# Kernel optimization log

Hardware: AMD Instinct MI355X
Metric: run time of the kernel (lower is better)

## Reference

```python
import jax, jax.numpy as jnp
import numpy as np
import math

D_MODEL = 1024
NUM_HEADS = 16
HEAD_DIM = D_MODEL // NUM_HEADS


def _xavier(key, out_f, in_f):
    limit = math.sqrt(6.0 / (in_f + out_f))
    return jax.random.uniform(key, (out_f, in_f), jnp.float32, -limit, limit)


def ternarize(w):
    # abs-mean threshold -> {-1, 0, +1}
    abs_mean = jnp.mean(jnp.abs(w))
    return jnp.where(jnp.abs(w) > abs_mean, jnp.sign(w), jnp.zeros_like(w))


def setup_inputs() -> dict:
    key = jax.random.key(0)
    kq, kk, kv, kwq, kwk, kwv, kwo = jax.random.split(key, 7)
    B, S = 2, 2048
    return {
        "query": jax.random.normal(kq, (B, S, D_MODEL), jnp.float32),
        "key": jax.random.normal(kk, (B, S, D_MODEL), jnp.float32),
        "value": jax.random.normal(kv, (B, S, D_MODEL), jnp.float32),
        "w_q": _xavier(kwq, D_MODEL, D_MODEL),
        "w_k": _xavier(kwk, D_MODEL, D_MODEL),
        "w_v": _xavier(kwv, D_MODEL, D_MODEL),
        "w_o": _xavier(kwo, D_MODEL, D_MODEL),
    }


def reference(query, key, value, w_q, w_k, w_v, w_o):
    B, S, _ = query.shape
    # ternary projections (F.linear: x @ W.T)
    q = query @ ternarize(w_q).T
    k = key @ ternarize(w_k).T
    v = value @ ternarize(w_v).T
    # [B, H, S, Dh]
    q = q.reshape(B, S, NUM_HEADS, HEAD_DIM).transpose(0, 2, 1, 3)
    k = k.reshape(B, -1, NUM_HEADS, HEAD_DIM).transpose(0, 2, 1, 3)
    v = v.reshape(B, -1, NUM_HEADS, HEAD_DIM).transpose(0, 2, 1, 3)
    scores = jnp.einsum("bhqd,bhkd->bhqk", q, k) / math.sqrt(HEAD_DIM)
    probs = jax.nn.softmax(scores, axis=-1)
    out = jnp.einsum("bhqk,bhkd->bhqd", probs, v)
    out = out.transpose(0, 2, 1, 3).reshape(B, S, D_MODEL)
    return out @ ternarize(w_o).T
```

## Files before the change

kernel.cpp:

```cpp
#include <hip/hip_runtime.h>
#include <cstdint>
#include <cstddef>

typedef __bf16 bfloat;
typedef __bf16 bf16x8 __attribute__((ext_vector_type(8)));
typedef __bf16 bf16x4 __attribute__((ext_vector_type(4)));
typedef float  f32x4  __attribute__((ext_vector_type(4)));

static constexpr int D  = 1024;
static constexpr int S  = 2048;
static constexpr int B  = 2;
static constexpr int H  = 16;
static constexpr int DH = 64;
static constexpr int M  = B * S;
static constexpr int WMAT_N = 1024 * 1024;

#define MFMA_BF16(a, b, c) __builtin_amdgcn_mfma_f32_16x16x32_bf16((a), (b), (c), 0, 0, 0)

__device__ __forceinline__ void gl_lds16(const void* g, void* l) {
  __builtin_amdgcn_global_load_lds(
      (const __attribute__((address_space(1))) void*)g,
      (__attribute__((address_space(3))) void*)l, 16, 0, 0);
}

__global__ void prep_kernel(const float* __restrict__ w0, const float* __restrict__ w1,
                            const float* __restrict__ w2, const float* __restrict__ w3,
                            const float* __restrict__ qx, const float* __restrict__ kx,
                            const float* __restrict__ vx, bfloat* __restrict__ qhi,
                            bfloat* __restrict__ qlo, bfloat* __restrict__ khi,
                            bfloat* __restrict__ klo, bfloat* __restrict__ vhi,
                            double* __restrict__ sums) {
  const int y = blockIdx.y;
  if (y < 4) {
    const float* w = (y == 0) ? w0 : (y == 1) ? w1 : (y == 2) ? w2 : w3;
    const float4* w4 = (const float4*)w;
    double s = 0.0;
    for (int i = blockIdx.x * blockDim.x + threadIdx.x; i < (WMAT_N / 4);
         i += gridDim.x * blockDim.x) {
      float4 v = w4[i];
      s += (double)fabsf(v.x) + (double)fabsf(v.y) + (double)fabsf(v.z) + (double)fabsf(v.w);
    }
    for (int off = 1; off < 64; off <<= 1) s += __shfl_xor(s, off, 64);
    __shared__ double ps[4];
    if ((threadIdx.x & 63) == 0) ps[threadIdx.x >> 6] = s;
    __syncthreads();
    if (threadIdx.x == 0) atomicAdd(&sums[y], ps[0] + ps[1] + ps[2] + ps[3]);
  } else {
    const int z = y - 4;
    const float* x = (z == 0) ? qx : (z == 1) ? kx : vx;
    bfloat* hi = (z == 0) ? qhi : (z == 1) ? khi : vhi;
    bfloat* lo = (z == 0) ? qlo : (z == 1) ? klo : nullptr;
    const int n8 = M * D / 8;
    const float4* x4 = (const float4*)x;
    for (int i = blockIdx.x * blockDim.x + threadIdx.x; i < n8;
         i += gridDim.x * blockDim.x) {
      float4 a = x4[2 * i], b = x4[2 * i + 1];
      float f[8] = {a.x, a.y, a.z, a.w, b.x, b.y, b.z, b.w};
      bf16x8 h;
#pragma unroll
      for (int j = 0; j < 8; j++) h[j] = (bfloat)f[j];
      *(bf16x8*)&hi[(size_t)i * 8] = h;
      if (z < 2) {
        bf16x8 l;
#pragma unroll
        for (int j = 0; j < 8; j++) l[j] = (bfloat)(f[j] - (float)h[j]);
        *(bf16x8*)&lo[(size_t)i * 8] = l;
      }
    }
  }
}

__global__ void tern_kernel(const float* __restrict__ w0, const float* __restrict__ w1,
                            const float* __restrict__ w2, const float* __restrict__ w3,
                            bfloat* __restrict__ o0, bfloat* __restrict__ o1,
                            bfloat* __restrict__ o2, bfloat* __restrict__ o3,
                            const double* __restrict__ sums) {
  int z = blockIdx.y;
  const float* w = (z == 0) ? w0 : (z == 1) ? w1 : (z == 2) ? w2 : w3;
  bfloat* o = (z == 0) ? o0 : (z == 1) ? o1 : (z == 2) ? o2 : o3;
  double thr = sums[z] * (1.0 / (double)WMAT_N);
  const float4* w4 = (const float4*)w;
  for (int i = blockIdx.x * blockDim.x + threadIdx.x; i < (WMAT_N / 4);
       i += gridDim.x * blockDim.x) {
    float4 v = w4[i];
    bf16x4 r;
    r[0] = (bfloat)(((double)fabsf(v.x) > thr) ? (v.x > 0.f ? 1.f : -1.f) : 0.f);
    r[1] = (bfloat)(((double)fabsf(v.y) > thr) ? (v.y > 0.f ? 1.f : -1.f) : 0.f);
    r[2] = (bfloat)(((double)fabsf(v.z) > thr) ? (v.z > 0.f ? 1.f : -1.f) : 0.f);
    r[3] = (bfloat)(((double)fabsf(v.w) > thr) ? (v.w > 0.f ? 1.f : -1.f) : 0.f);
    *(bf16x4*)&o[(size_t)i * 4] = r;
  }
}

__global__ __launch_bounds__(256) void qkv_gemm(
    const bfloat* __restrict__ xqh, const bfloat* __restrict__ xql,
    const bfloat* __restrict__ xkh, const bfloat* __restrict__ xkl,
    const bfloat* __restrict__ xvh, const bfloat* __restrict__ wqt,
    const bfloat* __restrict__ wkt, const bfloat* __restrict__ wvt,
    bfloat* __restrict__ qmh, bfloat* __restrict__ qml,
    bfloat* __restrict__ kmh, bfloat* __restrict__ kml, bfloat* __restrict__ vtr) {
  constexpr int K = D;
  constexpr int N = D;
  __shared__ __align__(16) bfloat As0[128 * 64];
  __shared__ __align__(16) bfloat As1[128 * 64];
  __shared__ __align__(16) bfloat Ws[128 * 64];

  const int z = blockIdx.z;
  const bfloat *A0, *A1 = nullptr, *Wm;
  bfloat *Oh = nullptr, *Ol = nullptr;
  float scale = 1.f;
  bool split;
  if (z == 0) {
    A0 = xqh; A1 = xql; Wm = wqt; Oh = qmh; Ol = qml;
    scale = 0.18033688f;
    split = true;
  } else if (z == 1) {
    A0 = xkh; A1 = xkl; Wm = wkt; Oh = kmh; Ol = kml; split = true;
  } else {
    A0 = xvh; Wm = wvt; split = false;
  }

  const int t = threadIdx.x;
  const int w = t >> 6, lane = t & 63;
  const int quad = lane >> 4, l16 = lane & 15;
  const int wm = w >> 1, wn = w & 1;
  const int m0 = blockIdx.y * 128, n0 = blockIdx.x * 128;

  f32x4 acc[4][4] = {};

  const int srr = lane >> 3;
  const int spc = lane & 7;

  for (int kk = 0; kk < K; kk += 64) {
#pragma unroll
    for (int g = 0; g < 4; g++) {
      int row = w * 32 + g * 8 + srr;
      int cl = spc ^ (row & 7);
      int lo = (w * 32 + g * 8) * 64;
      gl_lds16(A0 + (size_t)(m0 + row) * K + kk + cl * 8, As0 + lo);
      if (split) gl_lds16(A1 + (size_t)(m0 + row) * K + kk + cl * 8, As1 + lo);
      gl_lds16(Wm + (size_t)(n0 + row) * K + kk + cl * 8, Ws + lo);
    }
    __syncthreads();

#pragma unroll
    for (int kidx = 0; kidx < 2; kidx++) {
      bf16x8 bfrag[4], afrag[4];
#pragma unroll
      for (int nt = 0; nt < 4; nt++) {
        int r = wn * 64 + nt * 16 + l16;
        bfrag[nt] = *(const bf16x8*)&Ws[r * 64 + (((kidx * 4 + quad) ^ (r & 7)) * 8)];
      }
#pragma unroll
      for (int mt = 0; mt < 4; mt++) {
        int r = wm * 64 + mt * 16 + l16;
        afrag[mt] = *(const bf16x8*)&As0[r * 64 + (((kidx * 4 + quad) ^ (r & 7)) * 8)];
      }
#pragma unroll
      for (int mt = 0; mt < 4; mt++)
#pragma unroll
        for (int nt = 0; nt < 4; nt++)
          acc[mt][nt] = MFMA_BF16(afrag[mt], bfrag[nt], acc[mt][nt]);
      if (split) {
#pragma unroll
        for (int mt = 0; mt < 4; mt++) {
          int r = wm * 64 + mt * 16 + l16;
          afrag[mt] = *(const bf16x8*)&As1[r * 64 + (((kidx * 4 + quad) ^ (r & 7)) * 8)];
        }
#pragma unroll
        for (int mt = 0; mt < 4; mt++)
#pragma unroll
          for (int nt = 0; nt < 4; nt++)
            acc[mt][nt] = MFMA_BF16(afrag[mt], bfrag[nt], acc[mt][nt]);
      }
    }
    __syncthreads();
  }

#pragma unroll
  for (int mt = 0; mt < 4; mt++) {
#pragma unroll
    for (int nt = 0; nt < 4; nt++) {
      const int row = m0 + wm * 64 + mt * 16 + quad * 4;
      const int col = n0 + wn * 64 + nt * 16 + l16;
      if (split) {
#pragma unroll
        for (int rg = 0; rg < 4; rg++) {
          float vv = acc[mt][nt][rg] * scale;
          size_t idx = (size_t)(row + rg) * N + col;
          bfloat hh = (bfloat)vv;
          Oh[idx] = hh;
          Ol[idx] = (bfloat)(vv - (float)hh);
        }
      } else {
        int bb = row >> 11, s = row & (S - 1);
        int kk6 = s & 63;
        int pos = (kk6 & 3) | (((kk6 >> 4) & 1) << 2) | (((kk6 >> 2) & 3) << 3) |
                  ((kk6 >> 5) << 5);
        int sp = (s & ~63) | pos;
        bf16x4 pk;
#pragma unroll
        for (int rg = 0; rg < 4; rg++) pk[rg] = (bfloat)acc[mt][nt][rg];
        *(bf16x4*)&vtr[(size_t)bb * D * S + (size_t)col * S + sp] = pk;
      }
    }
  }
}

__global__ __launch_bounds__(256, 4) void gemm_wo(const bfloat* __restrict__ A,
                                                  const bfloat* __restrict__ Wm,
                                                  float* __restrict__ Cf) {
  constexpr int K = D;
  constexpr int N = D;
  __shared__ __align__(16) bfloat As[64 * 64];
  __shared__ __align__(16) bfloat Ws[64 * 64];

  const int t = threadIdx.x;
  const int w = t >> 6, lane = t & 63;
  const int quad = lane >> 4, l16 = lane & 15;
  const int wm = w >> 1, wn = w & 1;
  const int m0 = blockIdx.y * 64, n0 = blockIdx.x * 64;

  f32x4 acc[2][2] = {};

  const int srr = lane >> 3;
  const int spc = lane & 7;

  for (int kk = 0; kk < K; kk += 64) {
#pragma unroll
    for (int g = 0; g < 2; g++) {
      int row = w * 16 + g * 8 + srr;
      int cl = spc ^ (row & 7);
      int lo = (w * 16 + g * 8) * 64;
      gl_lds16(A + (size_t)(m0 + row) * K + kk + cl * 8, As + lo);
      gl_lds16(Wm + (size_t)(n0 + row) * K + kk + cl * 8, Ws + lo);
    }
    __syncthreads();

#pragma unroll
    for (int kidx = 0; kidx < 2; kidx++) {
      bf16x8 af[2], bfr[2];
#pragma unroll
      for (int i = 0; i < 2; i++) {
        int ar = wm * 32 + i * 16 + l16;
        af[i] = *(const bf16x8*)&As[ar * 64 + (((kidx * 4 + quad) ^ (ar & 7)) * 8)];
        int br = wn * 32 + i * 16 + l16;
        bfr[i] = *(const bf16x8*)&Ws[br * 64 + (((kidx * 4 + quad) ^ (br & 7)) * 8)];
      }
#pragma unroll
      for (int mt = 0; mt < 2; mt++)
#pragma unroll
        for (int nt = 0; nt < 2; nt++)
          acc[mt][nt] = MFMA_BF16(af[mt], bfr[nt], acc[mt][nt]);
    }
    __syncthreads();
  }

#pragma unroll
  for (int mt = 0; mt < 2; mt++) {
#pragma unroll
    for (int nt = 0; nt < 2; nt++) {
      const int row = m0 + wm * 32 + mt * 16 + quad * 4;
      const int col = n0 + wn * 32 + nt * 16 + l16;
#pragma unroll
      for (int rg = 0; rg < 4; rg++) Cf[(size_t)(row + rg) * N + col] = acc[mt][nt][rg];
    }
  }
}

__global__ __launch_bounds__(256) void flash_kernel(
    const bfloat* __restrict__ qh, const bfloat* __restrict__ ql,
    const bfloat* __restrict__ kh, const bfloat* __restrict__ kl,
    const bfloat* __restrict__ vt, bfloat* __restrict__ outp) {
  __shared__ __align__(16) bfloat SM[20480];

  const int tid = threadIdx.x;
  const int w = tid >> 6, lane = tid & 63;
  const int quad = lane >> 4, l16 = lane & 15;

  const int blk = blockIdx.x;
  const int xcd = blk & 7, slot = blk >> 3;
  const int g = xcd * 4 + (slot >> 4);
  const int h = g & 15, b = g >> 4;
  const int q0 = (slot & 15) * 128;

  const size_t base = (size_t)b * S * D + (size_t)h * DH;
  const size_t vbase = (size_t)b * D * S + (size_t)h * DH * S;

  const int ssr = lane >> 3;
  const int spc = lane & 7;
  const int c8 = (spc ^ ssr) * 8;
  const int stKV = w * 1024;

  const bfloat* pKh = kh + base + (size_t)(w * 16 + ssr) * D + c8;
  const bfloat* pKl = kl + base + (size_t)(w * 16 + ssr) * D + c8;
  const bfloat* pV = vt + vbase + (size_t)(w * 16 + ssr) * S + c8;

  bf16x8 ones;
#pragma unroll
  for (int j = 0; j < 8; j++) ones[j] = (bfloat)1.f;

  {
    const bfloat* pQh = qh + base + (size_t)(q0 + w * 32 + ssr) * D + c8;
    const bfloat* pQl = ql + base + (size_t)(q0 + w * 32 + ssr) * D + c8;
#pragma unroll
    for (int gq = 0; gq < 4; gq++) {
      gl_lds16(pQh + gq * 8 * D, SM + w * 2048 + gq * 512);
      gl_lds16(pQl + gq * 8 * D, SM + 8192 + w * 2048 + gq * 512);
    }
  }
  asm volatile("s_waitcnt vmcnt(0)" ::: "memory");
  __builtin_amdgcn_s_barrier();
  asm volatile("" ::: "memory");

  const int fo0 = l16 * 64 + ((quad ^ (l16 & 7)) * 8);
  const int fo4 = fo0 ^ 32;

  bf16x8 qhf[2][2], qlf[2][2];
#pragma unroll
  for (int qs = 0; qs < 2; qs++) {
    const int fq = w * 2048 + qs * 1024;
    qhf[qs][0] = *(const bf16x8*)&SM[fq + fo0];
    qhf[qs][1] = *(const bf16x8*)&SM[fq + fo4];
    qlf[qs][0] = *(const bf16x8*)&SM[8192 + fq + fo0];
    qlf[qs][1] = *(const bf16x8*)&SM[8192 + fq + fo4];
  }
  asm volatile("s_waitcnt lgkmcnt(0)" ::: "memory");
  __builtin_amdgcn_s_barrier();
  asm volatile("" ::: "memory");

  gl_lds16(pKh, SM + 0 + stKV);
  gl_lds16(pKh + 8 * D, SM + 0 + stKV + 512);
  gl_lds16(pKl, SM + 4096 + stKV);
  gl_lds16(pKl + 8 * D, SM + 4096 + stKV + 512);
  pKh += 64 * D;
  pKl += 64 * D;
  asm volatile("s_waitcnt vmcnt(0)" ::: "memory");

  f32x4 Oa[2][4] = {};
  f32x4 La[2] = {};
  float m_i[2] = {-3.0e38f, -3.0e38f};
  constexpr int NT = S / 64;

  for (int t = 0; t < NT; ++t) {
    __builtin_amdgcn_s_barrier();
    asm volatile("" ::: "memory");
    const int cur = (t & 1) * 8192;
    const int nxt = 8192 - cur;

    gl_lds16(pV, SM + 16384 + stKV);
    gl_lds16(pV + 8 * S, SM + 16384 + stKV + 512);
    pV += 64;
    if (t < NT - 1) {
      gl_lds16(pKh, SM + nxt + stKV);
      gl_lds16(pKh + 8 * D, SM + nxt + stKV + 512);
      gl_lds16(pKl, SM + nxt + 4096 + stKV);
      gl_lds16(pKl + 8 * D, SM + nxt + 4096 + stKV + 512);
      pKh += 64 * D;
      pKl += 64 * D;
    }

    f32x4 sf[2][4];
    __builtin_amdgcn_s_setprio(1);
#pragma unroll
    for (int mt = 0; mt < 4; mt++) {
      bf16x8 bh0 = *(const bf16x8*)&SM[cur + fo0 + mt * 1024];
      bf16x8 bl0 = *(const bf16x8*)&SM[cur + 4096 + fo0 + mt * 1024];
      bf16x8 bh1 = *(const bf16x8*)&SM[cur + fo4 + mt * 1024];
      bf16x8 bl1 = *(const bf16x8*)&SM[cur + 4096 + fo4 + mt * 1024];
#pragma unroll
      for (int qs = 0; qs < 2; qs++) {
        f32x4 a = {};
        a = MFMA_BF16(bh0, qhf[qs][0], a);
        a = MFMA_BF16(bl0, qhf[qs][0], a);
        a = MFMA_BF16(bh0, qlf[qs][0], a);
        a = MFMA_BF16(bh1, qhf[qs][1], a);
        a = MFMA_BF16(bl1, qhf[qs][1], a);
        a = MFMA_BF16(bh1, qlf[qs][1], a);
        sf[qs][mt] = a;
      }
    }
    __builtin_amdgcn_s_setprio(0);

#pragma unroll
    for (int qs = 0; qs < 2; qs++) {
      float t0 = fmaxf(fmaxf(sf[qs][0][0], sf[qs][0][1]), fmaxf(sf[qs][0][2], sf[qs][0][3]));
      float t1 = fmaxf(fmaxf(sf[qs][1][0], sf[qs][1][1]), fmaxf(sf[qs][1][2], sf[qs][1][3]));
      float t2 = fmaxf(fmaxf(sf[qs][2][0], sf[qs][2][1]), fmaxf(sf[qs][2][2], sf[qs][2][3]));
      float t3 = fmaxf(fmaxf(sf[qs][3][0], sf[qs][3][1]), fmaxf(sf[qs][3][2], sf[qs][3][3]));
      float mm = fmaxf(fmaxf(t0, t1), fmaxf(t2, t3));
      mm = fmaxf(mm, __shfl_xor(mm, 16, 64));
      mm = fmaxf(mm, __shfl_xor(mm, 32, 64));
      if (__ballot(mm > m_i[qs] + 8.0f)) {
        float mnew = fmaxf(m_i[qs], mm);
        float alpha = exp2f(m_i[qs] - mnew);
        m_i[qs] = mnew;
#pragma unroll
        for (int mt = 0; mt < 4; mt++) Oa[qs][mt] *= alpha;
        La[qs] *= alpha;
      }
#pragma unroll
      for (int mt = 0; mt < 4; mt++)
#pragma unroll
        for (int rg = 0; rg < 4; rg++) sf[qs][mt][rg] = exp2f(sf[qs][mt][rg] - m_i[qs]);
    }

    if (t < NT - 1)
      asm volatile("s_waitcnt vmcnt(4)" ::: "memory");
    else
      asm volatile("s_waitcnt vmcnt(0)" ::: "memory");
    __builtin_amdgcn_s_barrier();
    asm volatile("" ::: "memory");

    __builtin_amdgcn_s_setprio(1);
#pragma unroll
    for (int kp = 0; kp < 2; kp++) {
      bf16x8 pb8[2];
#pragma unroll
      for (int qs = 0; qs < 2; qs++) {
#pragma unroll
        for (int rg = 0; rg < 4; rg++) {
          pb8[qs][rg] = (bfloat)sf[qs][2 * kp][rg];
          pb8[qs][4 + rg] = (bfloat)sf[qs][2 * kp + 1][rg];
        }
        La[qs] = MFMA_BF16(ones, pb8[qs], La[qs]);
      }
      const int fv = kp ? fo4 : fo0;
#pragma unroll
      for (int mt = 0; mt < 4; mt++) {
        bf16x8 va = *(const bf16x8*)&SM[16384 + fv + mt * 1024];
        Oa[0][mt] = MFMA_BF16(va, pb8[0], Oa[0][mt]);
        Oa[1][mt] = MFMA_BF16(va, pb8[1], Oa[1][mt]);
      }
    }
    __builtin_amdgcn_s_setprio(0);
    asm volatile("s_waitcnt vmcnt(0)" ::: "memory");
  }

#pragma unroll
  for (int qs = 0; qs < 2; qs++) {
    float inv = 1.0f / La[qs][0];
    const int qrow = q0 + w * 32 + qs * 16 + l16;
#pragma unroll
    for (int mt = 0; mt < 4; mt++) {
      bf16x4 ov;
#pragma unroll
      for (int rg = 0; rg < 4; rg++) ov[rg] = (bfloat)(Oa[qs][mt][rg] * inv);
      *(bf16x4*)&outp[base + (size_t)qrow * D + mt * 16 + quad * 4] = ov;
    }
  }
}

extern "C" void kernel_launch(void* const* d_in, const int* in_sizes, int n_in,
                              void* d_out, int out_size, void* d_ws, size_t ws_size,
                              hipStream_t stream) {
  const float* q_in = (const float*)d_in[0];
  const float* k_in = (const float*)d_in[1];
  const float* v_in = (const float*)d_in[2];
  const float* wq = (const float*)d_in[3];
  const float* wk = (const float*)d_in[4];
  const float* wv = (const float*)d_in[5];
  const float* wo = (const float*)d_in[6];
  float* outp = (float*)d_out;
  char* ws = (char*)d_ws;

  constexpr size_t WBYTES = (size_t)WMAT_N * 2;
  constexpr size_t XBYTES = (size_t)M * D * 2;
  size_t off = 0;
  double* sums = (double*)(ws + off); off += 256;
  bfloat* wqt = (bfloat*)(ws + off); off += WBYTES;
  bfloat* wkt = (bfloat*)(ws + off); off += WBYTES;
  bfloat* wvt = (bfloat*)(ws + off); off += WBYTES;
  bfloat* wot = (bfloat*)(ws + off); off += WBYTES;
  bfloat* xqh = (bfloat*)(ws + off); off += XBYTES;
  bfloat* xql = (bfloat*)(ws + off); off += XBYTES;
  bfloat* xkh = (bfloat*)(ws + off); off += XBYTES;
  bfloat* xkl = (bfloat*)(ws + off); off += XBYTES;
  bfloat* xvh = (bfloat*)(ws + off); off += XBYTES;
  bfloat* qmh = (bfloat*)(ws + off); off += XBYTES;
  bfloat* qml = (bfloat*)(ws + off); off += XBYTES;
  bfloat* kmh = (bfloat*)(ws + off); off += XBYTES;
  bfloat* kml = (bfloat*)(ws + off); off += XBYTES;
  bfloat* vtr = (bfloat*)(ws + off); off += XBYTES;
  bfloat* attn = xqh;

  hipMemsetAsync(sums, 0, 4 * sizeof(double), stream);
  prep_kernel<<<dim3(256, 7), 256, 0, stream>>>(
      wq, wk, wv, wo, q_in, k_in, v_in, xqh, xql, xkh, xkl, xvh, sums);
  tern_kernel<<<dim3(128, 4), 256, 0, stream>>>(wq, wk, wv, wo, wqt, wkt, wvt, wot, sums);
  qkv_gemm<<<dim3(D / 128, M / 128, 3), 256, 0, stream>>>(
      xqh, xql, xkh, xkl, xvh, wqt, wkt, wvt, qmh, qml, kmh, kml, vtr);
  flash_kernel<<<512, 256, 0, stream>>>(qmh, qml, kmh, kml, vtr, attn);
  gemm_wo<<<dim3(D / 64, M / 64), 256, 0, stream>>>(attn, wot, outp);
}
```

Measured before the change: 291.1 us.

## Split flash attention KV range across two wave groups per block and merge

```diff
diff --git a/kernel.cpp b/kernel.cpp
--- a/kernel.cpp
+++ b/kernel.cpp
@@ -268,21 +268,23 @@
   }
 }
 
-__global__ __launch_bounds__(256) void flash_kernel(
+__global__ __launch_bounds__(512, 4) void flash_kernel(
     const bfloat* __restrict__ qh, const bfloat* __restrict__ ql,
     const bfloat* __restrict__ kh, const bfloat* __restrict__ kl,
     const bfloat* __restrict__ vt, bfloat* __restrict__ outp) {
-  __shared__ __align__(16) bfloat SM[20480];
+  __shared__ __align__(16) bfloat SM[24576];
 
   const int tid = threadIdx.x;
   const int w = tid >> 6, lane = tid & 63;
   const int quad = lane >> 4, l16 = lane & 15;
+  const int p = w >> 2;
+  const int wq4 = w & 3;
 
   const int blk = blockIdx.x;
-  const int xcd = blk & 7, slot = blk >> 3;
-  const int g = xcd * 4 + (slot >> 4);
+  const int xcd = blk & 7, bs = blk >> 3;
+  const int g = xcd * 4 + (bs >> 4);
   const int h = g & 15, b = g >> 4;
-  const int q0 = (slot & 15) * 128;
+  const int q0 = (bs & 15) * 128;
 
   const size_t base = (size_t)b * S * D + (size_t)h * DH;
   const size_t vbase = (size_t)b * D * S + (size_t)h * DH * S;
@@ -290,24 +292,23 @@
   const int ssr = lane >> 3;
   const int spc = lane & 7;
   const int c8 = (spc ^ ssr) * 8;
-  const int stKV = w * 1024;
-
-  const bfloat* pKh = kh + base + (size_t)(w * 16 + ssr) * D + c8;
-  const bfloat* pKl = kl + base + (size_t)(w * 16 + ssr) * D + c8;
-  const bfloat* pV = vt + vbase + (size_t)(w * 16 + ssr) * S + c8;
+  const int stKV = w * 512;
+
+  const bfloat* pKh = kh + base + (size_t)(w * 8 + ssr) * D + c8;
+  const bfloat* pKl = kl + base + (size_t)(w * 8 + ssr) * D + c8;
+  const bfloat* pV = vt + vbase + (size_t)(w * 8 + ssr) * S + c8;
 
   bf16x8 ones;
 #pragma unroll
   for (int j = 0; j < 8; j++) ones[j] = (bfloat)1.f;
 
   {
-    const bfloat* pQh = qh + base + (size_t)(q0 + w * 32 + ssr) * D + c8;
-    const bfloat* pQl = ql + base + (size_t)(q0 + w * 32 + ssr) * D + c8;
-#pragma unroll
-    for (int gq = 0; gq < 4; gq++) {
-      gl_lds16(pQh + gq * 8 * D, SM + w * 2048 + gq * 512);
-      gl_lds16(pQl + gq * 8 * D, SM + 8192 + w * 2048 + gq * 512);
-    }
+    const bfloat* pQh = qh + base + (size_t)(q0 + w * 16 + ssr) * D + c8;
+    const bfloat* pQl = ql + base + (size_t)(q0 + w * 16 + ssr) * D + c8;
+    gl_lds16(pQh, SM + w * 1024);
+    gl_lds16(pQh + 8 * D, SM + w * 1024 + 512);
+    gl_lds16(pQl, SM + 8192 + w * 1024);
+    gl_lds16(pQl + 8 * D, SM + 8192 + w * 1024 + 512);
   }
   asm volatile("s_waitcnt vmcnt(0)" ::: "memory");
   __builtin_amdgcn_s_barrier();
@@ -319,7 +320,7 @@
   bf16x8 qhf[2][2], qlf[2][2];
 #pragma unroll
   for (int qs = 0; qs < 2; qs++) {
-    const int fq = w * 2048 + qs * 1024;
+    const int fq = wq4 * 2048 + qs * 1024;
     qhf[qs][0] = *(const bf16x8*)&SM[fq + fo0];
     qhf[qs][1] = *(const bf16x8*)&SM[fq + fo4];
     qlf[qs][0] = *(const bf16x8*)&SM[8192 + fq + fo0];
@@ -330,44 +331,37 @@
   asm volatile("" ::: "memory");
 
   gl_lds16(pKh, SM + 0 + stKV);
-  gl_lds16(pKh + 8 * D, SM + 0 + stKV + 512);
   gl_lds16(pKl, SM + 4096 + stKV);
-  gl_lds16(pKl + 8 * D, SM + 4096 + stKV + 512);
-  pKh += 64 * D;
-  pKl += 64 * D;
-  asm volatile("s_waitcnt vmcnt(0)" ::: "memory");
+  gl_lds16(pKh + 64 * D, SM + 8192 + stKV);
+  gl_lds16(pKl + 64 * D, SM + 12288 + stKV);
+  gl_lds16(pV, SM + 16384 + stKV);
+  gl_lds16(pV + 64, SM + 20480 + stKV);
+  pKh += 128 * D;
+  pKl += 128 * D;
+  pV += 128;
+
+  const int kH = p ? 8192 : 0;
+  const int kL = kH + 4096;
+  const int vb = 16384 + p * 4096;
 
   f32x4 Oa[2][4] = {};
   f32x4 La[2] = {};
   float m_i[2] = {-3.0e38f, -3.0e38f};
-  constexpr int NT = S / 64;
-
-  for (int t = 0; t < NT; ++t) {
+  constexpr int NS = S / 128;
+
+  for (int s = 0; s < NS; ++s) {
+    asm volatile("s_waitcnt vmcnt(2)" ::: "memory");
     __builtin_amdgcn_s_barrier();
     asm volatile("" ::: "memory");
-    const int cur = (t & 1) * 8192;
-    const int nxt = 8192 - cur;
-
-    gl_lds16(pV, SM + 16384 + stKV);
-    gl_lds16(pV + 8 * S, SM + 16384 + stKV + 512);
-    pV += 64;
-    if (t < NT - 1) {
-      gl_lds16(pKh, SM + nxt + stKV);
-      gl_lds16(pKh + 8 * D, SM + nxt + stKV + 512);
-      gl_lds16(pKl, SM + nxt + 4096 + stKV);
-      gl_lds16(pKl + 8 * D, SM + nxt + 4096 + stKV + 512);
-      pKh += 64 * D;
-      pKl += 64 * D;
-    }
 
     f32x4 sf[2][4];
     __builtin_amdgcn_s_setprio(1);
 #pragma unroll
     for (int mt = 0; mt < 4; mt++) {
-      bf16x8 bh0 = *(const bf16x8*)&SM[cur + fo0 + mt * 1024];
-      bf16x8 bl0 = *(const bf16x8*)&SM[cur + 4096 + fo0 + mt * 1024];
-      bf16x8 bh1 = *(const bf16x8*)&SM[cur + fo4 + mt * 1024];
-      bf16x8 bl1 = *(const bf16x8*)&SM[cur + 4096 + fo4 + mt * 1024];
+      bf16x8 bh0 = *(const bf16x8*)&SM[kH + fo0 + mt * 1024];
+      bf16x8 bl0 = *(const bf16x8*)&SM[kL + fo0 + mt * 1024];
+      bf16x8 bh1 = *(const bf16x8*)&SM[kH + fo4 + mt * 1024];
+      bf16x8 bl1 = *(const bf16x8*)&SM[kL + fo4 + mt * 1024];
 #pragma unroll
       for (int qs = 0; qs < 2; qs++) {
         f32x4 a = {};
@@ -405,12 +399,18 @@
         for (int rg = 0; rg < 4; rg++) sf[qs][mt][rg] = exp2f(sf[qs][mt][rg] - m_i[qs]);
     }
 
-    if (t < NT - 1)
-      asm volatile("s_waitcnt vmcnt(4)" ::: "memory");
-    else
-      asm volatile("s_waitcnt vmcnt(0)" ::: "memory");
+    asm volatile("s_waitcnt vmcnt(0)" ::: "memory");
     __builtin_amdgcn_s_barrier();
     asm volatile("" ::: "memory");
+
+    if (s < NS - 1) {
+      gl_lds16(pKh, SM + 0 + stKV);
+      gl_lds16(pKl, SM + 4096 + stKV);
+      gl_lds16(pKh + 64 * D, SM + 8192 + stKV);
+      gl_lds16(pKl + 64 * D, SM + 12288 + stKV);
+      pKh += 128 * D;
+      pKl += 128 * D;
+    }
 
     __builtin_amdgcn_s_setprio(1);
 #pragma unroll
@@ -428,25 +428,60 @@
       const int fv = kp ? fo4 : fo0;
 #pragma unroll
       for (int mt = 0; mt < 4; mt++) {
-        bf16x8 va = *(const bf16x8*)&SM[16384 + fv + mt * 1024];
+        bf16x8 va = *(const bf16x8*)&SM[vb + fv + mt * 1024];
         Oa[0][mt] = MFMA_BF16(va, pb8[0], Oa[0][mt]);
         Oa[1][mt] = MFMA_BF16(va, pb8[1], Oa[1][mt]);
       }
     }
     __builtin_amdgcn_s_setprio(0);
-    asm volatile("s_waitcnt vmcnt(0)" ::: "memory");
-  }
-
-#pragma unroll
-  for (int qs = 0; qs < 2; qs++) {
-    float inv = 1.0f / La[qs][0];
-    const int qrow = q0 + w * 32 + qs * 16 + l16;
-#pragma unroll
-    for (int mt = 0; mt < 4; mt++) {
-      bf16x4 ov;
-#pragma unroll
-      for (int rg = 0; rg < 4; rg++) ov[rg] = (bfloat)(Oa[qs][mt][rg] * inv);
-      *(bf16x4*)&outp[base + (size_t)qrow * D + mt * 16 + quad * 4] = ov;
+
+    __builtin_amdgcn_s_barrier();
+    asm volatile("" ::: "memory");
+
+    if (s < NS - 1) {
+      gl_lds16(pV, SM + 16384 + stKV);
+      gl_lds16(pV + 64, SM + 20480 + stKV);
+      pV += 128;
+    }
+  }
+
+  float* FP = (float*)SM;
+  const int slot = (wq4 * 64 + lane) * 32;
+  const int sb = 8192 + (wq4 * 64 + lane) * 4;
+  if (p == 0) {
+#pragma unroll
+    for (int qs = 0; qs < 2; qs++)
+#pragma unroll
+      for (int mt = 0; mt < 4; mt++)
+        *(f32x4*)&FP[slot + qs * 16 + mt * 4] = Oa[qs][mt];
+    FP[sb + 0] = m_i[0];
+    FP[sb + 1] = La[0][0];
+    FP[sb + 2] = m_i[1];
+    FP[sb + 3] = La[1][0];
+  }
+  asm volatile("s_waitcnt lgkmcnt(0)" ::: "memory");
+  __builtin_amdgcn_s_barrier();
+  asm volatile("" ::: "memory");
+  if (p == 1) {
+#pragma unroll
+    for (int qs = 0; qs < 2; qs++) {
+      float m_e = FP[sb + qs * 2];
+      float l_e = FP[sb + qs * 2 + 1];
+      float m_c = fmaxf(m_e, m_i[qs]);
+      float ae = exp2f(m_e - m_c);
+      float ao = exp2f(m_i[qs] - m_c);
+      float l = l_e * ae + La[qs][0] * ao;
+      float inv = 1.0f / l;
+      const int qrow = q0 + wq4 * 32 + qs * 16 + l16;
+#pragma unroll
+      for (int mt = 0; mt < 4; mt++) {
+        f32x4 oe = *(const f32x4*)&FP[slot + qs * 16 + mt * 4];
+        bf16x4 ov;
+#pragma unroll
+        for (int rg = 0; rg < 4; rg++)
+          ov[rg] = (bfloat)((oe[rg] * ae + Oa[qs][mt][rg] * ao) * inv);
+        *(bf16x4*)&outp[base + (size_t)qrow * D + mt * 16 + quad * 4] = ov;
+      }
     }
   }
 }
@@ -490,6 +525,6 @@
   tern_kernel<<<dim3(128, 4), 256, 0, stream>>>(wq, wk, wv, wo, wqt, wkt, wvt, wot, sums);
   qkv_gemm<<<dim3(D / 128, M / 128, 3), 256, 0, stream>>>(
       xqh, xql, xkh, xkl, xvh, wqt, wkt, wvt, qmh, qml, kmh, kml, vtr);
-  flash_kernel<<<512, 256, 0, stream>>>(qmh, qml, kmh, kml, vtr, attn);
+  flash_kernel<<<512, 512, 0, stream>>>(qmh, qml, kmh, kml, vtr, attn);
   gemm_wo<<<dim3(D / 64, M / 64), 256, 0, stream>>>(attn, wot, outp);
 }
```

Measured after the change: 345.6 us. +18.7%, slower.
